# Optimization experiments

Measured on AMD Instinct MI355X. Metric: run time of the kernel, lower is better.

## Reference

```python
import jax, jax.numpy as jnp
import numpy as np

D = 2048
H = 16
HD = 128
INNER = H * HD
EPS = 1e-6


def rmsnorm(x, w):
    var = jnp.mean(x * x, axis=-1, keepdims=True)
    return x * jax.lax.rsqrt(var + EPS) * w


def setup_inputs() -> dict:
    key = jax.random.key(0)
    ks = jax.random.split(key, 10)
    B, T, N_ws, T_corr = 2, 2048, 64, 512
    scale = 1.0 / np.sqrt(D)
    return {
        "hidden_states": jax.random.normal(ks[0], (B, T, D), jnp.float32),
        "workspace": jax.random.normal(ks[1], (B, N_ws, D), jnp.float32),
        "correction_tokens": jax.random.normal(ks[2], (B, T_corr, D), jnp.float32),
        "correction_mask": jax.random.randint(ks[3], (B, T_corr), 0, 2, jnp.int32),
        "ln_q_w": jnp.ones((D,), jnp.float32),
        "ln_kv_w": jnp.ones((D,), jnp.float32),
        "Wq": jax.random.normal(ks[4], (D, INNER), jnp.float32) * scale,
        "Wk": jax.random.normal(ks[5], (D, INNER), jnp.float32) * scale,
        "Wv": jax.random.normal(ks[6], (D, INNER), jnp.float32) * scale,
        "Wo": jax.random.normal(ks[7], (INNER, D), jnp.float32) * scale,
    }


def reference(hidden_states, workspace, correction_tokens, correction_mask,
              ln_q_w, ln_kv_w, Wq, Wk, Wv, Wo):
    B, T, _ = hidden_states.shape
    N_ws = workspace.shape[1]
    # kv context = [workspace ; correction_tokens]
    kv_context = jnp.concatenate([workspace, correction_tokens], axis=1)  # (B, N_kv, D)
    N_kv = kv_context.shape[1]
    ws_mask = jnp.ones((B, N_ws), hidden_states.dtype)
    kv_mask = jnp.concatenate([ws_mask, correction_mask.astype(hidden_states.dtype)], axis=1)  # (B, N_kv)

    h = rmsnorm(hidden_states, ln_q_w)
    kv = rmsnorm(kv_context, ln_kv_w)

    q = (h @ Wq).reshape(B, T, H, HD)        # (B,T,H,hd)
    k = (kv @ Wk).reshape(B, N_kv, H, HD)
    v = (kv @ Wv).reshape(B, N_kv, H, HD)

    scores = jnp.einsum("bthd,bshd->bhts", q, k) / np.sqrt(HD)  # (B,H,T,N_kv)
    mask = (kv_mask != 0)[:, None, None, :]                      # (B,1,1,N_kv)
    scores = jnp.where(mask, scores, -jnp.inf)
    attn = jax.nn.softmax(scores, axis=-1)
    attn = jnp.nan_to_num(attn, nan=0.0)
    # dropout is identity in eval mode
    out = jnp.einsum("bhts,bshd->bthd", attn, v).reshape(B, T, INNER)
    return out @ Wo
```

## Files before the change

### kernel.cpp

```cpp
#include <hip/hip_runtime.h>
#include <hip/hip_bf16.h>
#include <math.h>

typedef __bf16 bf16;
typedef __attribute__((ext_vector_type(8))) __bf16 bf16x8;
typedef __attribute__((ext_vector_type(4))) __bf16 bf16x4;
typedef __attribute__((ext_vector_type(4))) float f32x4;

#define D_DIM 2048
#define NKV   576

__device__ inline void gld_lds16(const void* g, void* l) {
    void* gg = const_cast<void*>(g);
    __builtin_amdgcn_global_load_lds(
        (__attribute__((address_space(1))) void*)gg,
        (__attribute__((address_space(3))) void*)l, 16, 0, 0);
}

#define PH_BARRIER() do { __builtin_amdgcn_s_barrier(); asm volatile("" ::: "memory"); } while (0)
#define VMCNT(n)     asm volatile("s_waitcnt vmcnt(" #n ")" ::: "memory")

__global__ __launch_bounds__(256) void prep(
    const float* __restrict__ hidden, const float* __restrict__ wsp,
    const float* __restrict__ corr, const float* __restrict__ lnq,
    const float* __restrict__ lnkv,
    const float* __restrict__ Wq, const float* __restrict__ Wk,
    const float* __restrict__ Wv, const float* __restrict__ Wo,
    bf16* __restrict__ hb, bf16* __restrict__ kvb,
    bf16* __restrict__ WqT, bf16* __restrict__ WkvT, bf16* __restrict__ WoT)
{
    __shared__ float tl[64][65];
    __shared__ float p[4];
    const int id = blockIdx.x, t = threadIdx.x;

    if (id < 4096) {
        const int wz = id >> 10, idx = id & 1023;
        const int wy = idx >> 5, wx = idx & 31;
        const float* in; bf16* out;
        switch (wz) {
            case 0:  in = Wq; out = WqT; break;
            case 1:  in = Wk; out = WkvT; break;
            case 2:  in = Wv; out = WkvT + 2048ull * 2048; break;
            default: in = Wo; out = WoT; break;
        }
        const int r0 = wy * 64, c0 = wx * 64;
        const int tr = t >> 4, tc = (t & 15) * 4;
#pragma unroll
        for (int q = 0; q < 4; ++q) {
            const int r = tr + q * 16;
            float4 v = *(const float4*)(in + (long)(r0 + r) * 2048 + c0 + tc);
            tl[r][tc] = v.x; tl[r][tc + 1] = v.y;
            tl[r][tc + 2] = v.z; tl[r][tc + 3] = v.w;
        }
        __syncthreads();
#pragma unroll
        for (int q = 0; q < 4; ++q) {
            const int orr = tr + q * 16;
            bf16x4 o = { (bf16)tl[tc][orr], (bf16)tl[tc + 1][orr],
                         (bf16)tl[tc + 2][orr], (bf16)tl[tc + 3][orr] };
            *(bf16x4*)(out + (long)(c0 + orr) * 2048 + r0 + tc) = o;
        }
        return;
    }

    const int rr0 = id - 4096;
    const float* xr; const float* w; bf16* yr;
    if (rr0 < 4096) {
        xr = hidden + (long)rr0 * D_DIM; w = lnq; yr = hb + (long)rr0 * D_DIM;
    } else if (rr0 < 4224) {
        const int rr = rr0 - 4096;
        xr = wsp + (long)rr * D_DIM; w = lnkv;
        yr = kvb + ((long)(rr >> 6) * NKV + (rr & 63)) * D_DIM;
    } else {
        const int rr = rr0 - 4224;
        xr = corr + (long)rr * D_DIM; w = lnkv;
        yr = kvb + ((long)(rr >> 9) * NKV + 64 + (rr & 511)) * D_DIM;
    }

    float4 v0 = *(const float4*)(xr + t * 4);
    float4 v1 = *(const float4*)(xr + 1024 + t * 4);
    float ss = v0.x * v0.x + v0.y * v0.y + v0.z * v0.z + v0.w * v0.w
             + v1.x * v1.x + v1.y * v1.y + v1.z * v1.z + v1.w * v1.w;
#pragma unroll
    for (int off = 32; off; off >>= 1) ss += __shfl_xor(ss, off);
    if ((t & 63) == 0) p[t >> 6] = ss;
    __syncthreads();
    const float rs = rsqrtf((p[0] + p[1] + p[2] + p[3]) * (1.0f / 2048.0f) + 1e-6f);

    float4 w0 = *(const float4*)(w + t * 4);
    float4 w1 = *(const float4*)(w + 1024 + t * 4);
    bf16x4 o0 = { (bf16)(v0.x * rs * w0.x), (bf16)(v0.y * rs * w0.y),
                  (bf16)(v0.z * rs * w0.z), (bf16)(v0.w * rs * w0.w) };
    bf16x4 o1 = { (bf16)(v1.x * rs * w1.x), (bf16)(v1.y * rs * w1.y),
                  (bf16)(v1.z * rs * w1.z), (bf16)(v1.w * rs * w1.w) };
    *(bf16x4*)(yr + t * 4) = o0;
    *(bf16x4*)(yr + 1024 + t * 4) = o1;
}

__global__ __launch_bounds__(512, 2) void proj_all(
    const bf16* __restrict__ hb, const bf16* __restrict__ kvb,
    const bf16* __restrict__ WqT, const bf16* __restrict__ WkvT,
    bf16* __restrict__ qb, bf16* __restrict__ kb, bf16* __restrict__ vtb)
{
    __shared__ __align__(16) bf16 smem[4][16384];
    bf16* const EA = smem[0]; bf16* const EB = smem[1];
    bf16* const OA = smem[2]; bf16* const OB = smem[3];

    const int id0 = blockIdx.x;
    const int id = (id0 & 7) * 26 + (id0 >> 3);
    const bf16 *A, *B; int m0, n0; bool isQ;
    if (id < 128) {
        isQ = true;  A = hb;  B = WqT;
        m0 = (id >> 3) * 256; n0 = (id & 7) * 256;
    } else {
        const int kd = id - 128;
        isQ = false; A = kvb; B = WkvT;
        m0 = (kd >> 4) * 256; n0 = (kd & 15) * 256;
    }

    const int tid = threadIdx.x, lane = tid & 63, w = tid >> 6;
    const int wm = (w >> 2) * 128, wn = (w & 3) * 64;
    const int fr = lane & 15, fg = lane >> 4;

    f32x4 acc[8][4] = {};
    bf16x8 af[4][2], bg[4][2];

    const int aoff0 = (wm + fr) * 64 + (fg ^ (fr & 7)) * 8;
    const int boff0 = (wn + fr) * 64 + (fg ^ (fr & 7)) * 8;
    const int aoff1 = aoff0 ^ 32, boff1 = boff0 ^ 32;
    const bf16* const pAE[2] = { EA + aoff0, EA + aoff1 };
    const bf16* const pAO[2] = { OA + aoff0, OA + aoff1 };
    const bf16* const pBE[2] = { EB + boff0, EB + boff1 };
    const bf16* const pBO[2] = { OB + boff0, OB + boff1 };

    const long toff = (long)(tid >> 3) * 2048 + (((tid & 7) ^ ((tid >> 3) & 7)) * 8);
    const bf16* const gA0 = A + (long)m0 * 2048 + toff;
    const bf16* const gA1 = gA0 + 262144;
    const bf16* const gB0 = B + (long)n0 * 2048 + toff;
    const bf16* const gB1 = gB0 + 262144;
    bf16* const dT = (bf16*)smem + tid * 8;

    auto stage2 = [&](const bf16* g, int k, int dslot) {
        gld_lds16(g + k, dT + dslot);
        gld_lds16(g + 131072 + k, dT + dslot + 4096);
    };
    enum { sEA0 = 0, sEA1 = 8192, sEB0 = 16384, sEB1 = 24576,
           sOA0 = 32768, sOA1 = 40960, sOB0 = 49152, sOB1 = 57344 };

    auto load_af = [&](const bf16* const p[2], int ib) {
#pragma unroll
        for (int i = 0; i < 4; ++i)
#pragma unroll
            for (int s = 0; s < 2; ++s)
                af[i][s] = *(const bf16x8*)(p[s] + (ib + i) * 1024);
    };
    auto load_bg = [&](const bf16* const p[2], int jb) {
#pragma unroll
        for (int j = 0; j < 2; ++j)
#pragma unroll
            for (int s = 0; s < 2; ++s)
                bg[jb + j][s] = *(const bf16x8*)(p[s] + (jb + j) * 1024);
    };
    auto mfma16 = [&](int ib, int jb) {
        __builtin_amdgcn_s_setprio(1);
#pragma unroll
        for (int s = 0; s < 2; ++s)
#pragma unroll
            for (int i = 0; i < 4; ++i)
#pragma unroll
                for (int j = 0; j < 2; ++j)
                    acc[ib + i][jb + j] = __builtin_amdgcn_mfma_f32_16x16x32_bf16(
                        af[i][s], bg[jb + j][s], acc[ib + i][jb + j], 0, 0, 0);
        __builtin_amdgcn_s_setprio(0);
    };

    stage2(gA0, 0, sEA0); stage2(gA1, 0, sEA1);
    stage2(gB0, 0, sEB0); stage2(gB1, 0, sEB1);
    stage2(gB0, 64, sOB0); stage2(gB1, 64, sOB1);
    VMCNT(4);
    PH_BARRIER();

    for (int it = 0; it < 15; ++it) {
        const int kO = it * 128 + 64, kE2 = it * 128 + 128, kO2 = it * 128 + 192;
        load_af(pAE, 0); load_bg(pBE, 0);
        stage2(gA0, kO, sOA0);
        PH_BARRIER(); mfma16(0, 0); PH_BARRIER();
        load_bg(pBE, 2);
        stage2(gA1, kO, sOA1);
        PH_BARRIER(); mfma16(0, 2); PH_BARRIER();
        load_af(pAE, 4);
        stage2(gB0, kE2, sEB0);
        PH_BARRIER(); mfma16(4, 2); PH_BARRIER();
        stage2(gB1, kE2, sEB1);
        PH_BARRIER(); mfma16(4, 0); VMCNT(4); PH_BARRIER();
        load_af(pAO, 0); load_bg(pBO, 0);
        stage2(gA0, kE2, sEA0);
        PH_BARRIER(); mfma16(0, 0); PH_BARRIER();
        load_bg(pBO, 2);
        stage2(gA1, kE2, sEA1);
        PH_BARRIER(); mfma16(0, 2); PH_BARRIER();
        load_af(pAO, 4);
        stage2(gB0, kO2, sOB0);
        PH_BARRIER(); mfma16(4, 2); PH_BARRIER();
        stage2(gB1, kO2, sOB1);
        PH_BARRIER(); mfma16(4, 0); VMCNT(4); PH_BARRIER();
    }
    {
        load_af(pAE, 0); load_bg(pBE, 0);
        stage2(gA0, 1984, sOA0);
        PH_BARRIER(); mfma16(0, 0); PH_BARRIER();
        load_bg(pBE, 2);
        stage2(gA1, 1984, sOA1);
        PH_BARRIER(); mfma16(0, 2); PH_BARRIER();
        load_af(pAE, 4);
        PH_BARRIER(); mfma16(4, 2); PH_BARRIER();
        PH_BARRIER(); mfma16(4, 0); VMCNT(0); PH_BARRIER();
        load_af(pAO, 0); load_bg(pBO, 0);
        PH_BARRIER(); mfma16(0, 0); PH_BARRIER();
        load_bg(pBO, 2);
        PH_BARRIER(); mfma16(0, 2); PH_BARRIER();
        load_af(pAO, 4);
        PH_BARRIER(); mfma16(4, 2); PH_BARRIER();
        PH_BARRIER(); mfma16(4, 0); PH_BARRIER();
    }

    __syncthreads();

    const int er = fg * 4;
    if (isQ || n0 < 2048) {
        bf16* C = isQ ? qb : kb;
        const int mlim = isQ ? 4096 : 1152;
#pragma unroll
        for (int i = 0; i < 8; ++i)
#pragma unroll
            for (int j = 0; j < 4; ++j) {
                const int n = n0 + wn + j * 16 + fr;
#pragma unroll
                for (int r = 0; r < 4; ++r) {
                    const int m = m0 + wm + i * 16 + er + r;
                    if (m < mlim)
                        C[(long)m * 2048 + n] = (bf16)acc[i][j][r];
                }
            }
        return;
    }

    bf16* T = &smem[0][0];
#pragma unroll
    for (int p2 = 0; p2 < 2; ++p2) {
        if (p2) __syncthreads();
        if ((wn >> 7) == p2) {
            const int nb = wn - p2 * 128;
#pragma unroll
            for (int i = 0; i < 8; ++i)
#pragma unroll
                for (int j = 0; j < 4; ++j) {
                    const int nl = nb + j * 16 + fr;
#pragma unroll
                    for (int r = 0; r < 4; ++r)
                        T[nl * 264 + wm + i * 16 + er + r] = (bf16)acc[i][j][r];
                }
        }
        __syncthreads();
        const int hh = (n0 - 2048 + p2 * 128) >> 7;
        for (int e = tid; e < 128 * 64; e += 512) {
            const int d = e >> 6, mg = (e & 63) * 4;
            const int mm = m0 + mg;
            if (mm < 1152) {
                bf16x4 val = *(const bf16x4*)(T + d * 264 + mg);
                const int bb = mm >= NKV;
                const int s = mm - bb * NKV;
                *(bf16x4*)(vtb + ((long)((bb * 16 + hh) * 128 + d)) * NKV + s) = val;
            }
        }
    }
}

__global__ __launch_bounds__(512, 2) void gemm_final(
    const bf16* __restrict__ Ag, const bf16* __restrict__ Bg, float* __restrict__ C)
{
    __shared__ __align__(16) bf16 smem[49152];
    bf16* const EA = smem;           bf16* const EB = smem + 16384;
    bf16* const OA = smem + 24576;   bf16* const OB = smem + 40960;

    const int id0 = blockIdx.x;
    const int id = (id0 & 7) * 32 + (id0 >> 3);
    const int m0 = (id >> 4) * 256, n0 = (id & 15) * 128;

    const int tid = threadIdx.x, lane = tid & 63, w = tid >> 6;
    const int wm = (w >> 1) * 64, wn = (w & 1) * 64;
    const int fr = lane & 15, fg = lane >> 4;

    f32x4 acc[4][4] = {};
    bf16x8 af[2][2], bg[4][2];

    const int aoff0 = (wm + fr) * 64 + (fg ^ (fr & 7)) * 8;
    const int boff0 = (wn + fr) * 64 + (fg ^ (fr & 7)) * 8;
    const int aoff1 = aoff0 ^ 32, boff1 = boff0 ^ 32;
    const bf16* const pAE[2] = { EA + aoff0, EA + aoff1 };
    const bf16* const pAO[2] = { OA + aoff0, OA + aoff1 };
    const bf16* const pBE[2] = { EB + boff0, EB + boff1 };
    const bf16* const pBO[2] = { OB + boff0, OB + boff1 };

    const long toff = (long)(tid >> 3) * 2048 + (((tid & 7) ^ ((tid >> 3) & 7)) * 8);
    const bf16* const gA0 = Ag + (long)m0 * 2048 + toff;
    const bf16* const gA1 = gA0 + 262144;
    const bf16* const gB0 = Bg + (long)n0 * 2048 + toff;
    bf16* const dT = smem + tid * 8;

    auto stage2 = [&](const bf16* g, int k, int dslot) {
        gld_lds16(g + k, dT + dslot);
        gld_lds16(g + 131072 + k, dT + dslot + 4096);
    };
    enum { sEA0 = 0, sEA1 = 8192, sEB0 = 16384,
           sOA0 = 24576, sOA1 = 32768, sOB0 = 40960 };

    auto load_af = [&](const bf16* const p[2], int ib) {
#pragma unroll
        for (int i = 0; i < 2; ++i)
#pragma unroll
            for (int s = 0; s < 2; ++s)
                af[i][s] = *(const bf16x8*)(p[s] + (ib + i) * 1024);
    };
    auto load_bg = [&](const bf16* const p[2], int jb) {
#pragma unroll
        for (int j = 0; j < 2; ++j)
#pragma unroll
            for (int s = 0; s < 2; ++s)
                bg[jb + j][s] = *(const bf16x8*)(p[s] + (jb + j) * 1024);
    };
    auto mfma8 = [&](int ib, int jb) {
        __builtin_amdgcn_s_setprio(1);
#pragma unroll
        for (int s = 0; s < 2; ++s)
#pragma unroll
            for (int i = 0; i < 2; ++i)
#pragma unroll
                for (int j = 0; j < 2; ++j)
                    acc[ib + i][jb + j] = __builtin_amdgcn_mfma_f32_16x16x32_bf16(
                        af[i][s], bg[jb + j][s], acc[ib + i][jb + j], 0, 0, 0);
        __builtin_amdgcn_s_setprio(0);
    };

    stage2(gA0, 0, sEA0); stage2(gA1, 0, sEA1);
    stage2(gB0, 0, sEB0);
    stage2(gB0, 64, sOB0);
    VMCNT(2);
    PH_BARRIER();

    for (int it = 0; it < 15; ++it) {
        const int kO = it * 128 + 64, kE2 = it * 128 + 128, kO2 = it * 128 + 192;
        load_af(pAE, 0); load_bg(pBE, 0);
        stage2(gA0, kO, sOA0);
        PH_BARRIER(); mfma8(0, 0); PH_BARRIER();
        load_bg(pBE, 2);
        stage2(gA1, kO, sOA1);
        PH_BARRIER(); mfma8(0, 2); PH_BARRIER();
        load_af(pAE, 2);
        stage2(gB0, kE2, sEB0);
        PH_BARRIER(); mfma8(2, 2); PH_BARRIER();
        stage2(gA0, kE2, sEA0);
        PH_BARRIER(); mfma8(2, 0); VMCNT(4); PH_BARRIER();
        load_af(pAO, 0); load_bg(pBO, 0);
        stage2(gA1, kE2, sEA1);
        PH_BARRIER(); mfma8(0, 0); PH_BARRIER();
        load_bg(pBO, 2);
        PH_BARRIER(); mfma8(0, 2); PH_BARRIER();
        load_af(pAO, 2);
        stage2(gB0, kO2, sOB0);
        PH_BARRIER(); mfma8(2, 2); PH_BARRIER();
        PH_BARRIER(); mfma8(2, 0); VMCNT(2); PH_BARRIER();
    }
    {
        load_af(pAE, 0); load_bg(pBE, 0);
        stage2(gA0, 1984, sOA0);
        PH_BARRIER(); mfma8(0, 0); PH_BARRIER();
        load_bg(pBE, 2);
        stage2(gA1, 1984, sOA1);
        PH_BARRIER(); mfma8(0, 2); PH_BARRIER();
        load_af(pAE, 2);
        PH_BARRIER(); mfma8(2, 2); PH_BARRIER();
        PH_BARRIER(); mfma8(2, 0); VMCNT(0); PH_BARRIER();
        load_af(pAO, 0); load_bg(pBO, 0);
        PH_BARRIER(); mfma8(0, 0); PH_BARRIER();
        load_bg(pBO, 2);
        PH_BARRIER(); mfma8(0, 2); PH_BARRIER();
        load_af(pAO, 2);
        PH_BARRIER(); mfma8(2, 2); PH_BARRIER();
        PH_BARRIER(); mfma8(2, 0); PH_BARRIER();
    }

    __syncthreads();

    const int er = fg * 4;
#pragma unroll
    for (int i = 0; i < 4; ++i)
#pragma unroll
        for (int j = 0; j < 4; ++j) {
            const int n = n0 + wn + j * 16 + fr;
#pragma unroll
            for (int r = 0; r < 4; ++r)
                C[(long)(m0 + wm + i * 16 + er + r) * 2048 + n] = acc[i][j][r];
        }
}

__global__ __launch_bounds__(256, 4) void flash_attn(
    const bf16* __restrict__ Q, const bf16* __restrict__ K,
    const bf16* __restrict__ VT, const int* __restrict__ cmask,
    bf16* __restrict__ O)
{
    __shared__ __align__(16) bf16 Ks[64 * 128];
    __shared__ __align__(16) bf16 VTs[128 * 64];

    const int qt = blockIdx.x, h = blockIdx.y, b = blockIdx.z;
    const int tid = threadIdx.x, lane = tid & 63, w = tid >> 6;
    const int fr = lane & 15, fg = lane >> 4;

    const bf16* qbase = Q + ((long)(b * 2048 + qt * 64)) * 2048 + h * 128;
    bf16x8 qf[4];
#pragma unroll
    for (int s = 0; s < 4; ++s)
        qf[s] = *(const bf16x8*)(qbase + (long)(w * 16 + fr) * 2048 + s * 32 + fg * 8);

    float m_r[4], l_r[4];
    f32x4 acc_o[8];
#pragma unroll
    for (int r = 0; r < 4; ++r) { m_r[r] = -3.0e38f; l_r[r] = 0.f; }
#pragma unroll
    for (int j = 0; j < 8; ++j) acc_o[j] = (f32x4){0.f, 0.f, 0.f, 0.f};

    const float scale2 = 0.12752792330124195f;
    const bf16* kbase = K + (long)b * NKV * 2048 + h * 128;
    const bf16* vbase = VT + ((long)(b * 16 + h)) * 128 * NKV;

    for (int kc = 0; kc < 9; ++kc) {
        const int kv0 = kc * 64;
#pragma unroll
        for (int p = 0; p < 4; ++p) {
            const int c = p * 256 + tid;
            const int r = c >> 4, cs = c & 15, cl = cs ^ (r & 15);
            gld_lds16(kbase + (long)(kv0 + r) * 2048 + cl * 8, Ks + c * 8);
        }
#pragma unroll
        for (int p = 0; p < 4; ++p) {
            const int c = p * 256 + tid;
            const int r = c >> 3, cs = c & 7, cl = cs ^ (r & 7);
            gld_lds16(vbase + (long)r * NKV + kv0 + cl * 8, VTs + c * 8);
        }
        __syncthreads();

        f32x4 acc_s[4] = {};
#pragma unroll
        for (int s = 0; s < 4; ++s) {
#pragma unroll
            for (int j = 0; j < 4; ++j) {
                bf16x8 bgv = *(const bf16x8*)(Ks +
                    ((j * 16 + fr) * 16 + ((s * 4 + fg) ^ fr)) * 8);
                acc_s[j] = __builtin_amdgcn_mfma_f32_16x16x32_bf16(qf[s], bgv, acc_s[j], 0, 0, 0);
            }
        }

        float bias[4];
#pragma unroll
        for (int j = 0; j < 4; ++j) {
            const int kv = kv0 + j * 16 + fr;
            const bool valid = (kv < 64) || (cmask[b * 512 + kv - 64] != 0);
            bias[j] = valid ? 0.f : -1e30f;
        }
        float s_f[4][4];
        float mc[4] = {-3.0e38f, -3.0e38f, -3.0e38f, -3.0e38f};
#pragma unroll
        for (int j = 0; j < 4; ++j)
#pragma unroll
            for (int r = 0; r < 4; ++r) {
                float v = fmaf(acc_s[j][r], scale2, bias[j]);
                s_f[j][r] = v; mc[r] = fmaxf(mc[r], v);
            }
#pragma unroll
        for (int r = 0; r < 4; ++r) {
            mc[r] = fmaxf(mc[r], __shfl_xor(mc[r], 1));
            mc[r] = fmaxf(mc[r], __shfl_xor(mc[r], 2));
            mc[r] = fmaxf(mc[r], __shfl_xor(mc[r], 4));
            mc[r] = fmaxf(mc[r], __shfl_xor(mc[r], 8));
        }
        float alpha[4];
#pragma unroll
        for (int r = 0; r < 4; ++r) {
            const float mn = fmaxf(m_r[r], mc[r]);
            alpha[r] = __builtin_amdgcn_exp2f(m_r[r] - mn);
            m_r[r] = mn;
        }
        float rs[4] = {0.f, 0.f, 0.f, 0.f};
#pragma unroll
        for (int j = 0; j < 4; ++j)
#pragma unroll
            for (int r = 0; r < 4; ++r) {
                const float pv = __builtin_amdgcn_exp2f(s_f[j][r] - m_r[r]);
                s_f[j][r] = pv; rs[r] += pv;
            }
#pragma unroll
        for (int r = 0; r < 4; ++r) {
            rs[r] += __shfl_xor(rs[r], 1);
            rs[r] += __shfl_xor(rs[r], 2);
            rs[r] += __shfl_xor(rs[r], 4);
            rs[r] += __shfl_xor(rs[r], 8);
            l_r[r] = l_r[r] * alpha[r] + rs[r];
        }
#pragma unroll
        for (int j = 0; j < 8; ++j)
#pragma unroll
            for (int r = 0; r < 4; ++r) acc_o[j][r] *= alpha[r];

        __syncthreads();

        bf16* Ps = Ks;
#pragma unroll
        for (int j = 0; j < 4; ++j)
#pragma unroll
            for (int r = 0; r < 4; ++r)
                Ps[(w * 16 + fg * 4 + r) * 72 + j * 16 + fr] = (bf16)s_f[j][r];

#pragma unroll
        for (int s2 = 0; s2 < 2; ++s2) {
            bf16x8 afv = *(const bf16x8*)(Ps + (w * 16 + fr) * 72 + s2 * 32 + fg * 8);
#pragma unroll
            for (int jd = 0; jd < 8; ++jd) {
                bf16x8 bgv = *(const bf16x8*)(VTs +
                    ((jd * 16 + fr) * 8 + ((s2 * 4 + fg) ^ (fr & 7))) * 8);
                acc_o[jd] = __builtin_amdgcn_mfma_f32_16x16x32_bf16(afv, bgv, acc_o[jd], 0, 0, 0);
            }
        }
        __syncthreads();
    }

    bf16* obase = O + ((long)(b * 2048 + qt * 64)) * 2048 + h * 128;
#pragma unroll
    for (int r = 0; r < 4; ++r) {
        const float inv = 1.0f / l_r[r];
        const int row = w * 16 + fg * 4 + r;
#pragma unroll
        for (int jd = 0; jd < 8; ++jd)
            obase[(long)row * 2048 + jd * 16 + fr] = (bf16)(acc_o[jd][r] * inv);
    }
}

extern "C" void kernel_launch(void* const* d_in, const int* in_sizes, int n_in,
                              void* d_out, int out_size, void* d_ws, size_t ws_size,
                              hipStream_t stream)
{
    const float* hidden = (const float*)d_in[0];
    const float* wsp    = (const float*)d_in[1];
    const float* corr   = (const float*)d_in[2];
    const int*   cmask  = (const int*)d_in[3];
    const float* lnq    = (const float*)d_in[4];
    const float* lnkv   = (const float*)d_in[5];
    const float* Wq     = (const float*)d_in[6];
    const float* Wk     = (const float*)d_in[7];
    const float* Wv     = (const float*)d_in[8];
    const float* Wo     = (const float*)d_in[9];
    float* out = (float*)d_out;

    char* ws = (char*)d_ws;
    size_t off = 0;
    auto alloc = [&](size_t sz) { void* p = ws + off; off += (sz + 255) & ~(size_t)255; return p; };

    bf16* WqT   = (bf16*)alloc(2048ull * 2048 * 2);
    bf16* WkvT  = (bf16*)alloc(4096ull * 2048 * 2);
    bf16* WoT   = (bf16*)alloc(2048ull * 2048 * 2);
    bf16* hb    = (bf16*)alloc(4096ull * 2048 * 2);
    bf16* kvb   = (bf16*)alloc(1280ull * 2048 * 2);
    bf16* qb    = (bf16*)alloc(4096ull * 2048 * 2);
    bf16* kb    = (bf16*)alloc(1152ull * 2048 * 2);
    bf16* vtb   = (bf16*)alloc(4096ull * NKV * 2);
    bf16* aob   = (bf16*)alloc(4096ull * 2048 * 2);

    prep<<<9344, 256, 0, stream>>>(hidden, wsp, corr, lnq, lnkv,
                                   Wq, Wk, Wv, Wo, hb, kvb, WqT, WkvT, WoT);
    proj_all<<<208, 512, 0, stream>>>(hb, kvb, WqT, WkvT, qb, kb, vtb);
    flash_attn<<<dim3(32, 16, 2), 256, 0, stream>>>(qb, kb, vtb, cmask, aob);
    gemm_final<<<256, 512, 0, stream>>>(aob, WoT, out);
}
```

Baseline: 298.2 us.

## Prefetch LDS fragments during MFMA phases in both GEMM kernels

The LDS-to-register fragment loads now sit inside the MFMA phases, after the mfma calls and before the barrier, instead of at the start of the next phase. The B fragments are loaded all at once (four columns) so the next half-tile's operands are in registers before its first MFMA. The vmcnt waits move earlier so the LDS data is ready when read. This aims to hide LDS read latency behind matrix math, at the cost of more live registers and a changed ordering between LDS reads and async global-to-LDS writes, which could race or hurt occupancy.

```diff
diff --git a/kernel.cpp b/kernel.cpp
--- a/kernel.cpp
+++ b/kernel.cpp
@@ -154,12 +154,12 @@
             for (int s = 0; s < 2; ++s)
                 af[i][s] = *(const bf16x8*)(p[s] + (ib + i) * 1024);
     };
-    auto load_bg = [&](const bf16* const p[2], int jb) {
-#pragma unroll
-        for (int j = 0; j < 2; ++j)
+    auto load_bg4 = [&](const bf16* const p[2]) {
+#pragma unroll
+        for (int j = 0; j < 4; ++j)
 #pragma unroll
             for (int s = 0; s < 2; ++s)
-                bg[jb + j][s] = *(const bf16x8*)(p[s] + (jb + j) * 1024);
+                bg[j][s] = *(const bf16x8*)(p[s] + j * 1024);
     };
     auto mfma16 = [&](int ib, int jb) {
         __builtin_amdgcn_s_setprio(1);
@@ -179,47 +179,36 @@
     stage2(gB0, 64, sOB0); stage2(gB1, 64, sOB1);
     VMCNT(4);
     PH_BARRIER();
+    load_af(pAE, 0); load_bg4(pBE);
 
     for (int it = 0; it < 15; ++it) {
         const int kO = it * 128 + 64, kE2 = it * 128 + 128, kO2 = it * 128 + 192;
-        load_af(pAE, 0); load_bg(pBE, 0);
         stage2(gA0, kO, sOA0);
         PH_BARRIER(); mfma16(0, 0); PH_BARRIER();
-        load_bg(pBE, 2);
         stage2(gA1, kO, sOA1);
-        PH_BARRIER(); mfma16(0, 2); PH_BARRIER();
-        load_af(pAE, 4);
+        PH_BARRIER(); mfma16(0, 2); load_af(pAE, 4); PH_BARRIER();
         stage2(gB0, kE2, sEB0);
-        PH_BARRIER(); mfma16(4, 2); PH_BARRIER();
+        PH_BARRIER(); mfma16(4, 2); VMCNT(2); PH_BARRIER();
         stage2(gB1, kE2, sEB1);
-        PH_BARRIER(); mfma16(4, 0); VMCNT(4); PH_BARRIER();
-        load_af(pAO, 0); load_bg(pBO, 0);
+        PH_BARRIER(); mfma16(4, 0); load_af(pAO, 0); load_bg4(pBO); PH_BARRIER();
         stage2(gA0, kE2, sEA0);
         PH_BARRIER(); mfma16(0, 0); PH_BARRIER();
-        load_bg(pBO, 2);
         stage2(gA1, kE2, sEA1);
-        PH_BARRIER(); mfma16(0, 2); PH_BARRIER();
-        load_af(pAO, 4);
+        PH_BARRIER(); mfma16(0, 2); load_af(pAO, 4); PH_BARRIER();
         stage2(gB0, kO2, sOB0);
-        PH_BARRIER(); mfma16(4, 2); PH_BARRIER();
+        PH_BARRIER(); mfma16(4, 2); VMCNT(2); PH_BARRIER();
         stage2(gB1, kO2, sOB1);
-        PH_BARRIER(); mfma16(4, 0); VMCNT(4); PH_BARRIER();
+        PH_BARRIER(); mfma16(4, 0); load_af(pAE, 0); load_bg4(pBE); PH_BARRIER();
     }
     {
-        load_af(pAE, 0); load_bg(pBE, 0);
         stage2(gA0, 1984, sOA0);
         PH_BARRIER(); mfma16(0, 0); PH_BARRIER();
-        load_bg(pBE, 2);
         stage2(gA1, 1984, sOA1);
-        PH_BARRIER(); mfma16(0, 2); PH_BARRIER();
-        load_af(pAE, 4);
-        PH_BARRIER(); mfma16(4, 2); PH_BARRIER();
-        PH_BARRIER(); mfma16(4, 0); VMCNT(0); PH_BARRIER();
-        load_af(pAO, 0); load_bg(pBO, 0);
+        PH_BARRIER(); mfma16(0, 2); load_af(pAE, 4); PH_BARRIER();
+        PH_BARRIER(); mfma16(4, 2); VMCNT(0); PH_BARRIER();
+        PH_BARRIER(); mfma16(4, 0); load_af(pAO, 0); load_bg4(pBO); PH_BARRIER();
         PH_BARRIER(); mfma16(0, 0); PH_BARRIER();
-        load_bg(pBO, 2);
-        PH_BARRIER(); mfma16(0, 2); PH_BARRIER();
-        load_af(pAO, 4);
+        PH_BARRIER(); mfma16(0, 2); load_af(pAO, 4); PH_BARRIER();
         PH_BARRIER(); mfma16(4, 2); PH_BARRIER();
         PH_BARRIER(); mfma16(4, 0); PH_BARRIER();
     }
@@ -322,12 +311,12 @@
             for (int s = 0; s < 2; ++s)
                 af[i][s] = *(const bf16x8*)(p[s] + (ib + i) * 1024);
     };
-    auto load_bg = [&](const bf16* const p[2], int jb) {
-#pragma unroll
-        for (int j = 0; j < 2; ++j)
+    auto load_bg4 = [&](const bf16* const p[2]) {
+#pragma unroll
+        for (int j = 0; j < 4; ++j)
 #pragma unroll
             for (int s = 0; s < 2; ++s)
-                bg[jb + j][s] = *(const bf16x8*)(p[s] + (jb + j) * 1024);
+                bg[j][s] = *(const bf16x8*)(p[s] + j * 1024);
     };
     auto mfma8 = [&](int ib, int jb) {
         __builtin_amdgcn_s_setprio(1);
@@ -347,45 +336,34 @@
     stage2(gB0, 64, sOB0);
     VMCNT(2);
     PH_BARRIER();
+    load_af(pAE, 0); load_bg4(pBE);
 
     for (int it = 0; it < 15; ++it) {
         const int kO = it * 128 + 64, kE2 = it * 128 + 128, kO2 = it * 128 + 192;
-        load_af(pAE, 0); load_bg(pBE, 0);
         stage2(gA0, kO, sOA0);
         PH_BARRIER(); mfma8(0, 0); PH_BARRIER();
-        load_bg(pBE, 2);
         stage2(gA1, kO, sOA1);
-        PH_BARRIER(); mfma8(0, 2); PH_BARRIER();
-        load_af(pAE, 2);
+        PH_BARRIER(); mfma8(0, 2); load_af(pAE, 2); PH_BARRIER();
         stage2(gB0, kE2, sEB0);
-        PH_BARRIER(); mfma8(2, 2); PH_BARRIER();
+        PH_BARRIER(); mfma8(2, 2); VMCNT(2); PH_BARRIER();
         stage2(gA0, kE2, sEA0);
-        PH_BARRIER(); mfma8(2, 0); VMCNT(4); PH_BARRIER();
-        load_af(pAO, 0); load_bg(pBO, 0);
+        PH_BARRIER(); mfma8(2, 0); load_af(pAO, 0); load_bg4(pBO); PH_BARRIER();
         stage2(gA1, kE2, sEA1);
         PH_BARRIER(); mfma8(0, 0); PH_BARRIER();
-        load_bg(pBO, 2);
-        PH_BARRIER(); mfma8(0, 2); PH_BARRIER();
-        load_af(pAO, 2);
+        PH_BARRIER(); mfma8(0, 2); load_af(pAO, 2); PH_BARRIER();
         stage2(gB0, kO2, sOB0);
-        PH_BARRIER(); mfma8(2, 2); PH_BARRIER();
-        PH_BARRIER(); mfma8(2, 0); VMCNT(2); PH_BARRIER();
+        PH_BARRIER(); mfma8(2, 2); VMCNT(2); PH_BARRIER();
+        PH_BARRIER(); mfma8(2, 0); load_af(pAE, 0); load_bg4(pBE); PH_BARRIER();
     }
     {
-        load_af(pAE, 0); load_bg(pBE, 0);
         stage2(gA0, 1984, sOA0);
         PH_BARRIER(); mfma8(0, 0); PH_BARRIER();
-        load_bg(pBE, 2);
         stage2(gA1, 1984, sOA1);
-        PH_BARRIER(); mfma8(0, 2); PH_BARRIER();
-        load_af(pAE, 2);
-        PH_BARRIER(); mfma8(2, 2); PH_BARRIER();
-        PH_BARRIER(); mfma8(2, 0); VMCNT(0); PH_BARRIER();
-        load_af(pAO, 0); load_bg(pBO, 0);
+        PH_BARRIER(); mfma8(0, 2); load_af(pAE, 2); PH_BARRIER();
+        PH_BARRIER(); mfma8(2, 2); VMCNT(0); PH_BARRIER();
+        PH_BARRIER(); mfma8(2, 0); load_af(pAO, 0); load_bg4(pBO); PH_BARRIER();
         PH_BARRIER(); mfma8(0, 0); PH_BARRIER();
-        load_bg(pBO, 2);
-        PH_BARRIER(); mfma8(0, 2); PH_BARRIER();
-        load_af(pAO, 2);
+        PH_BARRIER(); mfma8(0, 2); load_af(pAO, 2); PH_BARRIER();
         PH_BARRIER(); mfma8(2, 2); PH_BARRIER();
         PH_BARRIER(); mfma8(2, 0); PH_BARRIER();
     }
```

Measured after the change: 299.3 us. About the same (+0.4%).

## Deepen global-to-LDS prefetch and load all B fragments up front in GEMMs

Applied to the files above, without the earlier changes.

In both the QKV and output-projection GEMM kernels, all four B-fragment reads from LDS now happen at the start of each half-iteration instead of being split into two. The global-to-LDS staging schedule is rotated so one more A tile is issued during the prologue, and the waitcnt thresholds are raised to keep more loads in flight. The goal is to hide global memory latency and LDS read latency better behind MFMA work. The cost is more live registers and a tighter dependence on the slot-reuse ordering being correct.

```diff
diff --git a/kernel.cpp b/kernel.cpp
--- a/kernel.cpp
+++ b/kernel.cpp
@@ -154,12 +154,12 @@
             for (int s = 0; s < 2; ++s)
                 af[i][s] = *(const bf16x8*)(p[s] + (ib + i) * 1024);
     };
-    auto load_bg = [&](const bf16* const p[2], int jb) {
-#pragma unroll
-        for (int j = 0; j < 2; ++j)
+    auto load_bg4 = [&](const bf16* const p[2]) {
+#pragma unroll
+        for (int j = 0; j < 4; ++j)
 #pragma unroll
             for (int s = 0; s < 2; ++s)
-                bg[jb + j][s] = *(const bf16x8*)(p[s] + (jb + j) * 1024);
+                bg[j][s] = *(const bf16x8*)(p[s] + j * 1024);
     };
     auto mfma16 = [&](int ib, int jb) {
         __builtin_amdgcn_s_setprio(1);
@@ -177,47 +177,43 @@
     stage2(gA0, 0, sEA0); stage2(gA1, 0, sEA1);
     stage2(gB0, 0, sEB0); stage2(gB1, 0, sEB1);
     stage2(gB0, 64, sOB0); stage2(gB1, 64, sOB1);
-    VMCNT(4);
+    stage2(gA0, 64, sOA0);
+    VMCNT(6);
     PH_BARRIER();
 
     for (int it = 0; it < 15; ++it) {
         const int kO = it * 128 + 64, kE2 = it * 128 + 128, kO2 = it * 128 + 192;
-        load_af(pAE, 0); load_bg(pBE, 0);
-        stage2(gA0, kO, sOA0);
+        load_af(pAE, 0); load_bg4(pBE);
+        stage2(gA1, kO, sOA1);
         PH_BARRIER(); mfma16(0, 0); PH_BARRIER();
-        load_bg(pBE, 2);
-        stage2(gA1, kO, sOA1);
+        stage2(gB0, kE2, sEB0);
         PH_BARRIER(); mfma16(0, 2); PH_BARRIER();
         load_af(pAE, 4);
-        stage2(gB0, kE2, sEB0);
+        stage2(gB1, kE2, sEB1);
         PH_BARRIER(); mfma16(4, 2); PH_BARRIER();
-        stage2(gB1, kE2, sEB1);
-        PH_BARRIER(); mfma16(4, 0); VMCNT(4); PH_BARRIER();
-        load_af(pAO, 0); load_bg(pBO, 0);
         stage2(gA0, kE2, sEA0);
+        PH_BARRIER(); mfma16(4, 0); VMCNT(6); PH_BARRIER();
+        load_af(pAO, 0); load_bg4(pBO);
+        stage2(gA1, kE2, sEA1);
         PH_BARRIER(); mfma16(0, 0); PH_BARRIER();
-        load_bg(pBO, 2);
-        stage2(gA1, kE2, sEA1);
+        stage2(gB0, kO2, sOB0);
         PH_BARRIER(); mfma16(0, 2); PH_BARRIER();
         load_af(pAO, 4);
-        stage2(gB0, kO2, sOB0);
+        stage2(gB1, kO2, sOB1);
         PH_BARRIER(); mfma16(4, 2); PH_BARRIER();
-        stage2(gB1, kO2, sOB1);
-        PH_BARRIER(); mfma16(4, 0); VMCNT(4); PH_BARRIER();
+        stage2(gA0, kO2, sOA0);
+        PH_BARRIER(); mfma16(4, 0); VMCNT(6); PH_BARRIER();
     }
     {
-        load_af(pAE, 0); load_bg(pBE, 0);
-        stage2(gA0, 1984, sOA0);
+        load_af(pAE, 0); load_bg4(pBE);
+        stage2(gA1, 1984, sOA1);
         PH_BARRIER(); mfma16(0, 0); PH_BARRIER();
-        load_bg(pBE, 2);
-        stage2(gA1, 1984, sOA1);
         PH_BARRIER(); mfma16(0, 2); PH_BARRIER();
         load_af(pAE, 4);
         PH_BARRIER(); mfma16(4, 2); PH_BARRIER();
         PH_BARRIER(); mfma16(4, 0); VMCNT(0); PH_BARRIER();
-        load_af(pAO, 0); load_bg(pBO, 0);
+        load_af(pAO, 0); load_bg4(pBO);
         PH_BARRIER(); mfma16(0, 0); PH_BARRIER();
-        load_bg(pBO, 2);
         PH_BARRIER(); mfma16(0, 2); PH_BARRIER();
         load_af(pAO, 4);
         PH_BARRIER(); mfma16(4, 2); PH_BARRIER();
@@ -322,12 +318,12 @@
             for (int s = 0; s < 2; ++s)
                 af[i][s] = *(const bf16x8*)(p[s] + (ib + i) * 1024);
     };
-    auto load_bg = [&](const bf16* const p[2], int jb) {
-#pragma unroll
-        for (int j = 0; j < 2; ++j)
+    auto load_bg4 = [&](const bf16* const p[2]) {
+#pragma unroll
+        for (int j = 0; j < 4; ++j)
 #pragma unroll
             for (int s = 0; s < 2; ++s)
-                bg[jb + j][s] = *(const bf16x8*)(p[s] + (jb + j) * 1024);
+                bg[j][s] = *(const bf16x8*)(p[s] + j * 1024);
     };
     auto mfma8 = [&](int ib, int jb) {
         __builtin_amdgcn_s_setprio(1);
@@ -344,46 +340,41 @@
 
     stage2(gA0, 0, sEA0); stage2(gA1, 0, sEA1);
     stage2(gB0, 0, sEB0);
-    stage2(gB0, 64, sOB0);
-    VMCNT(2);
+    stage2(gB0, 64, sOB0); stage2(gA0, 64, sOA0);
+    VMCNT(4);
     PH_BARRIER();
 
     for (int it = 0; it < 15; ++it) {
         const int kO = it * 128 + 64, kE2 = it * 128 + 128, kO2 = it * 128 + 192;
-        load_af(pAE, 0); load_bg(pBE, 0);
-        stage2(gA0, kO, sOA0);
+        load_af(pAE, 0); load_bg4(pBE);
+        stage2(gA1, kO, sOA1);
         PH_BARRIER(); mfma8(0, 0); PH_BARRIER();
-        load_bg(pBE, 2);
-        stage2(gA1, kO, sOA1);
+        stage2(gB0, kE2, sEB0);
         PH_BARRIER(); mfma8(0, 2); PH_BARRIER();
         load_af(pAE, 2);
-        stage2(gB0, kE2, sEB0);
         PH_BARRIER(); mfma8(2, 2); PH_BARRIER();
         stage2(gA0, kE2, sEA0);
         PH_BARRIER(); mfma8(2, 0); VMCNT(4); PH_BARRIER();
-        load_af(pAO, 0); load_bg(pBO, 0);
+        load_af(pAO, 0); load_bg4(pBO);
         stage2(gA1, kE2, sEA1);
         PH_BARRIER(); mfma8(0, 0); PH_BARRIER();
-        load_bg(pBO, 2);
+        stage2(gB0, kO2, sOB0);
         PH_BARRIER(); mfma8(0, 2); PH_BARRIER();
         load_af(pAO, 2);
-        stage2(gB0, kO2, sOB0);
         PH_BARRIER(); mfma8(2, 2); PH_BARRIER();
-        PH_BARRIER(); mfma8(2, 0); VMCNT(2); PH_BARRIER();
+        stage2(gA0, kO2, sOA0);
+        PH_BARRIER(); mfma8(2, 0); VMCNT(4); PH_BARRIER();
     }
     {
-        load_af(pAE, 0); load_bg(pBE, 0);
-        stage2(gA0, 1984, sOA0);
+        load_af(pAE, 0); load_bg4(pBE);
+        stage2(gA1, 1984, sOA1);
         PH_BARRIER(); mfma8(0, 0); PH_BARRIER();
-        load_bg(pBE, 2);
-        stage2(gA1, 1984, sOA1);
         PH_BARRIER(); mfma8(0, 2); PH_BARRIER();
         load_af(pAE, 2);
         PH_BARRIER(); mfma8(2, 2); PH_BARRIER();
         PH_BARRIER(); mfma8(2, 0); VMCNT(0); PH_BARRIER();
-        load_af(pAO, 0); load_bg(pBO, 0);
+        load_af(pAO, 0); load_bg4(pBO);
         PH_BARRIER(); mfma8(0, 0); PH_BARRIER();
-        load_bg(pBO, 2);
         PH_BARRIER(); mfma8(0, 2); PH_BARRIER();
         load_af(pAO, 2);
         PH_BARRIER(); mfma8(2, 2); PH_BARRIER();
```

After: 296.6 us. Within noise of the previous version (-0.5%).
